# Kernel optimization log

Measured on AMD Instinct MI355X. Metric: run time of the kernel, lower is better.

The kernel has to match this reference:

```python
import math
import jax, jax.numpy as jnp
import numpy as np

FACTOR = 3  # AutoCorrelation(factor=3)

def reference(queries, keys, values):
    # queries/keys/values: [B, L, D]; source requires L == S for the broadcast below.
    B, L, D = queries.shape
    S = keys.shape[1]
    # NOTE (faithful to source): rfft is over the LAST axis with fft_length L/S,
    # i.e. the feature axis D is zero-padded (or truncated) to length L.
    q_fft = jnp.fft.rfft(queries, n=L, axis=-1)          # [B, L, L//2+1] complex
    k_fft = jnp.fft.rfft(keys, n=S, axis=-1)             # [B, S, S//2+1] complex
    corr = jnp.fft.irfft(q_fft * jnp.conj(k_fft), n=L + S - 1, axis=-1)  # [B, L, L+S-1]

    top_k = int(FACTOR * math.log(float(L)))
    mean_value = jnp.mean(corr, axis=1)                  # [B, L+S-1]
    top_k = min(top_k, mean_value.shape[-1])
    top_k_val, top_k_ind = jax.lax.top_k(mean_value, top_k)  # [B, K]
    tmp_corr = jax.nn.softmax(top_k_val, axis=-1)        # [B, K]

    # Faithful to source: the roll shift for every batch element uses the
    # delays of batch element 0 (index[0] in the TF loop).
    shifts = top_k_ind[0]                                # [K] int32
    # Vectorized replacement of the per-index tf.roll loop.
    V_rolled = jax.vmap(lambda s: jnp.roll(values, -s, axis=1))(shifts)  # [K, B, L, D]
    # Weighted aggregation over the K retained delays (intended semantics of
    # the source einsum, which as written has a rank mismatch).
    output = jnp.einsum('kbld,bk->bld', V_rolled, tmp_corr)  # [B, L, D]
    return output

def setup_inputs() -> dict:
    key = jax.random.key(0)
    k1, k2, k3 = jax.random.split(key, 3)
    B, L, D = 8, 1024, 512
    return {
        'queries': jax.random.normal(k1, (B, L, D), dtype=jnp.float32),
        'keys':    jax.random.normal(k2, (B, L, D), dtype=jnp.float32),
        'values':  jax.random.normal(k3, (B, L, D), dtype=jnp.float32),
    }
```

## Files before the change

### kernel.cpp

```cpp
#include <hip/hip_runtime.h>
#include <math.h>

#define NB 8
#define NL 1024
#define ND 512
#define NF 513
#define NT 2047
#define TOPK 20

typedef __attribute__((ext_vector_type(8))) short short8;
typedef __attribute__((ext_vector_type(4))) float f32x4;

static __device__ __forceinline__ unsigned short bf16_rne(float x) {
    unsigned int u = __builtin_bit_cast(unsigned int, x);
    unsigned int r = (u + 0x7fffu + ((u >> 16) & 1u)) >> 16;
    return (unsigned short)r;
}
static __device__ __forceinline__ float bf16_to_f(unsigned short h) {
    unsigned int u = ((unsigned int)h) << 16;
    return __builtin_bit_cast(float, u);
}

__global__ __launch_bounds__(256) void k_tr(const float* __restrict__ q,
                                            const float* __restrict__ kk,
                                            unsigned short* __restrict__ Thi,
                                            unsigned short* __restrict__ Tlo,
                                            float* __restrict__ S) {
    __shared__ float tile[64][65];
    const int which = blockIdx.z;
    const int b  = blockIdx.y;
    const int l0 = (blockIdx.x & 15) * 64;
    const int d0 = (blockIdx.x >> 4) * 64;
    const int t = threadIdx.x;
    if (which == 0 && blockIdx.x == 0) {
        for (int i = t; i < 1023; i += 256) S[b * 1023 + i] = 0.f;
    }
    const float* src = (which ? kk : q) + (size_t)b * NL * ND;
    const int r = t >> 4, c = t & 15;
    #pragma unroll
    for (int rr = 0; rr < 4; ++rr) {
        const float4 v = *(const float4*)&src[(size_t)(l0 + r + 16 * rr) * ND + d0 + c * 4];
        tile[r + 16 * rr][c * 4 + 0] = v.x;
        tile[r + 16 * rr][c * 4 + 1] = v.y;
        tile[r + 16 * rr][c * 4 + 2] = v.z;
        tile[r + 16 * rr][c * 4 + 3] = v.w;
    }
    __syncthreads();
    unsigned short* hi = Thi + ((size_t)which * NB + b) * (size_t)ND * NL;
    unsigned short* lo = Tlo + ((size_t)which * NB + b) * (size_t)ND * NL;
    #pragma unroll
    for (int p = 0; p < 2; ++p) {
        const int c2 = t + 256 * p;
        const int dl = c2 >> 3;
        const int l8 = (c2 & 7) * 8;
        short8 vh, vl;
        #pragma unroll
        for (int i = 0; i < 8; ++i) {
            const float x = tile[l8 + i][dl];
            const unsigned short h = bf16_rne(x);
            vh[i] = (short)h;
            vl[i] = (short)bf16_rne(x - bf16_to_f(h));
        }
        *(short8*)&hi[(size_t)(d0 + dl) * NL + l0 + l8] = vh;
        *(short8*)&lo[(size_t)(d0 + dl) * NL + l0 + l8] = vl;
    }
}

#define GBK 32
#define GPAD 8
#define GKT 4

__global__ __launch_bounds__(256, 3) void k_gemm(const unsigned short* __restrict__ Thi,
                                                 const unsigned short* __restrict__ Tlo,
                                                 float* __restrict__ S) {
    __shared__ unsigned short Ahi[128][GBK + GPAD];
    __shared__ unsigned short Alo[128][GBK + GPAD];
    __shared__ unsigned short Bhi[128][GBK + GPAD];
    __shared__ unsigned short Blo[128][GBK + GPAD];
    __shared__ float sd4[4][256];
    const int id   = blockIdx.x;
    const int b    = id & 7;
    const int rest = id >> 3;
    const int mt = rest & 3, nt = (rest >> 2) & 3, kq = rest >> 4;
    const int tid  = threadIdx.x;
    const int lane = tid & 63, w = tid >> 6;
    const int wr = w >> 1, wc = w & 1;
    const int m = lane & 15, g = lane >> 4;

    const size_t plane = (size_t)ND * NL;
    const unsigned short* qhi = Thi + (size_t)b * plane;
    const unsigned short* khi = Thi + ((size_t)NB + b) * plane;
    const unsigned short* qlo = Tlo + (size_t)b * plane;
    const unsigned short* klo = Tlo + ((size_t)NB + b) * plane;

    f32x4 acc[4][4];
    #pragma unroll
    for (int i = 0; i < 4; ++i)
        #pragma unroll
        for (int j = 0; j < 4; ++j) acc[i][j] = (f32x4)(0.f);

    const int kbase = kq * GKT;
    short8 r_ah[2], r_al[2], r_bh[2], r_bl[2];
    #pragma unroll
    for (int p = 0; p < 2; ++p) {
        const int cc  = tid + 256 * p;
        const int row = cc >> 2, col8 = (cc & 3) * 8;
        const size_t ga = (size_t)(mt * 128 + row) * NL + kbase * GBK + col8;
        const size_t gb = (size_t)(nt * 128 + row) * NL + kbase * GBK + col8;
        r_ah[p] = *(const short8*)&qhi[ga];
        r_al[p] = *(const short8*)&qlo[ga];
        r_bh[p] = *(const short8*)&khi[gb];
        r_bl[p] = *(const short8*)&klo[gb];
    }

    for (int kt = 0; kt < GKT; ++kt) {
        __syncthreads();
        #pragma unroll
        for (int p = 0; p < 2; ++p) {
            const int cc  = tid + 256 * p;
            const int row = cc >> 2, col8 = (cc & 3) * 8;
            *(short8*)&Ahi[row][col8] = r_ah[p];
            *(short8*)&Alo[row][col8] = r_al[p];
            *(short8*)&Bhi[row][col8] = r_bh[p];
            *(short8*)&Blo[row][col8] = r_bl[p];
        }
        __syncthreads();
        if (kt + 1 < GKT) {
            #pragma unroll
            for (int p = 0; p < 2; ++p) {
                const int cc  = tid + 256 * p;
                const int row = cc >> 2, col8 = (cc & 3) * 8;
                const size_t ga = (size_t)(mt * 128 + row) * NL + (kbase + kt + 1) * GBK + col8;
                const size_t gb = (size_t)(nt * 128 + row) * NL + (kbase + kt + 1) * GBK + col8;
                r_ah[p] = *(const short8*)&qhi[ga];
                r_al[p] = *(const short8*)&qlo[ga];
                r_bh[p] = *(const short8*)&khi[gb];
                r_bl[p] = *(const short8*)&klo[gb];
            }
        }
        short8 ah[4], al[4], bh[4], bl[4];
        #pragma unroll
        for (int i = 0; i < 4; ++i) {
            ah[i] = *(const short8*)&Ahi[wr * 64 + i * 16 + m][g * 8];
            al[i] = *(const short8*)&Alo[wr * 64 + i * 16 + m][g * 8];
        }
        #pragma unroll
        for (int j = 0; j < 4; ++j) {
            bh[j] = *(const short8*)&Bhi[wc * 64 + j * 16 + m][g * 8];
            bl[j] = *(const short8*)&Blo[wc * 64 + j * 16 + m][g * 8];
        }
        #pragma unroll
        for (int i = 0; i < 4; ++i)
            #pragma unroll
            for (int j = 0; j < 4; ++j) {
                acc[i][j] = __builtin_amdgcn_mfma_f32_16x16x32_bf16(ah[i], bh[j], acc[i][j], 0, 0, 0);
                acc[i][j] = __builtin_amdgcn_mfma_f32_16x16x32_bf16(ah[i], bl[j], acc[i][j], 0, 0, 0);
                acc[i][j] = __builtin_amdgcn_mfma_f32_16x16x32_bf16(al[i], bh[j], acc[i][j], 0, 0, 0);
            }
    }

    for (int i = tid; i < 1024; i += 256) ((float*)sd4)[i] = 0.f;
    __syncthreads();
    float bin[7][4];
    #pragma unroll
    for (int u = 0; u < 7; ++u)
        #pragma unroll
        for (int r2 = 0; r2 < 4; ++r2) bin[u][r2] = 0.f;
    #pragma unroll
    for (int i = 0; i < 4; ++i)
        #pragma unroll
        for (int j = 0; j < 4; ++j)
            #pragma unroll
            for (int r2 = 0; r2 < 4; ++r2) bin[i - j + 3][r2] += acc[i][j][r2];
    const int basei = (wr - wc) * 64 + g * 4 - m + 127;
    #pragma unroll
    for (int u = 0; u < 7; ++u)
        #pragma unroll
        for (int r2 = 0; r2 < 4; ++r2)
            atomicAdd(&sd4[w][basei + (u - 3) * 16 + r2], bin[u][r2]);
    __syncthreads();
    const int doff = (mt - nt) * 128 + 511 - 127;
    if (tid < 255) {
        const float vsum = sd4[0][tid] + sd4[1][tid] + sd4[2][tid] + sd4[3][tid];
        atomicAdd(&S[b * 1023 + doff + tid], vsum);
    }
}

__global__ __launch_bounds__(64) void k_pdft(const float* __restrict__ S,
                                             float* __restrict__ pbar) {
    const int b = blockIdx.y;
    const int f = blockIdx.x;
    const int lane = threadIdx.x;
    const float w = 2.0f * 3.14159265358979323846f / 1024.0f;
    float re = 0.f, im = 0.f;
    #pragma unroll
    for (int i = 0; i < 16; ++i) {
        const int j = lane + 64 * i;
        if (j < 1023) {
            const int mm = (f * (j - 511)) & 1023;
            float s, c;
            sincosf(w * (float)mm, &s, &c);
            const float x = S[b * 1023 + j];
            re = fmaf(x, c, re);
            im = fmaf(x, -s, im);
        }
    }
    #pragma unroll
    for (int off = 32; off; off >>= 1) {
        re += __shfl_xor(re, off);
        im += __shfl_xor(im, off);
    }
    if (lane == 0) {
        pbar[b * 2 * NF + 2 * f]     = re;
        pbar[b * 2 * NF + 2 * f + 1] = im;
    }
}

__global__ __launch_bounds__(256) void k_mean(const float* __restrict__ pbar,
                                              float* __restrict__ mv) {
    __shared__ float P[2 * NF];
    const int b = blockIdx.y;
    for (int i = threadIdx.x; i < 2 * NF; i += 256)
        P[i] = pbar[(size_t)b * (2 * NF) + i];
    __syncthreads();
    const int wave = threadIdx.x >> 6, lane = threadIdx.x & 63;
    const int t = blockIdx.x * 4 + wave;
    if (t >= NT) return;
    const float w2 = 2.0f * 3.14159265358979323846f / 2047.0f;
    float acc = 0.f;
    #pragma unroll
    for (int i = 0; i < 8; ++i) {
        const int f = 1 + lane + 64 * i;
        const int mm = (f * t) % 2047;
        float s, c;
        sincosf(w2 * (float)mm, &s, &c);
        acc = fmaf(P[2 * f], c, acc);
        acc = fmaf(-P[2 * f + 1], s, acc);
    }
    acc *= 2.0f;
    #pragma unroll
    for (int off = 32; off; off >>= 1) acc += __shfl_xor(acc, off);
    if (lane == 0)
        mv[(size_t)b * NT + t] = (acc + P[0]) * (1.0f / (2047.0f * 1024.0f));
}

__global__ __launch_bounds__(256) void k_topk(const float* __restrict__ mv,
                                              float* __restrict__ wts,
                                              int* __restrict__ shifts) {
    __shared__ float v[NT];
    __shared__ float topv[TOPK];
    __shared__ int   topi[TOPK];
    __shared__ float wv[4];
    __shared__ int   wi[4];
    const int b = blockIdx.x;
    const int t = threadIdx.x;
    const int lane = t & 63, wave = t >> 6;
    for (int i = t; i < NT; i += 256) v[i] = mv[(size_t)b * NT + i];
    __syncthreads();
    for (int kkk = 0; kkk < TOPK; ++kkk) {
        float bv = -INFINITY; int bi = 0x7fffffff;
        #pragma unroll
        for (int s = 0; s < 8; ++s) {
            const int i = t + 256 * s;
            if (i < NT) {
                const float x = v[i];
                if (x > bv) { bv = x; bi = i; }
            }
        }
        #pragma unroll
        for (int off = 32; off; off >>= 1) {
            const float ov = __shfl_down(bv, off);
            const int   oi = __shfl_down(bi, off);
            if (ov > bv || (ov == bv && oi < bi)) { bv = ov; bi = oi; }
        }
        if (lane == 0) { wv[wave] = bv; wi[wave] = bi; }
        __syncthreads();
        if (t == 0) {
            bv = wv[0]; bi = wi[0];
            #pragma unroll
            for (int ww = 1; ww < 4; ++ww)
                if (wv[ww] > bv || (wv[ww] == bv && wi[ww] < bi)) { bv = wv[ww]; bi = wi[ww]; }
            topv[kkk] = bv; topi[kkk] = bi;
            v[bi] = -INFINITY;
        }
        __syncthreads();
    }
    if (t == 0) {
        float m = topv[0], sum = 0.f, e[TOPK];
        #pragma unroll
        for (int i = 0; i < TOPK; ++i) { e[i] = expf(topv[i] - m); sum += e[i]; }
        #pragma unroll
        for (int i = 0; i < TOPK; ++i) wts[b * TOPK + i] = e[i] / sum;
        if (b == 0) {
            #pragma unroll
            for (int i = 0; i < TOPK; ++i) shifts[i] = topi[i];
        }
    }
}

__global__ __launch_bounds__(128) void k_out(const float* __restrict__ vals,
                                             const float* __restrict__ wts,
                                             const int* __restrict__ shifts,
                                             float* __restrict__ out) {
    __shared__ float w[TOPK];
    __shared__ int   sh[TOPK];
    const int id = blockIdx.x;
    const int b = id & 7;
    const int l = id >> 3;
    const int t = threadIdx.x;
    if (t < TOPK) { w[t] = wts[b * TOPK + t]; sh[t] = shifts[t]; }
    __syncthreads();
    float4 acc = make_float4(0.f, 0.f, 0.f, 0.f);
    const float4* vb = (const float4*)(vals + (size_t)b * NL * ND);
    #pragma unroll 4
    for (int kkk = 0; kkk < TOPK; ++kkk) {
        const int sl = (l + sh[kkk]) & (NL - 1);
        const float4 x = vb[(size_t)sl * (ND / 4) + t];
        const float wk = w[kkk];
        acc.x = fmaf(wk, x.x, acc.x);
        acc.y = fmaf(wk, x.y, acc.y);
        acc.z = fmaf(wk, x.z, acc.z);
        acc.w = fmaf(wk, x.w, acc.w);
    }
    ((float4*)out)[((size_t)b * NL + l) * (ND / 4) + t] = acc;
}

extern "C" void kernel_launch(void* const* d_in, const int* in_sizes, int n_in,
                              void* d_out, int out_size, void* d_ws, size_t ws_size,
                              hipStream_t stream) {
    const float* q = (const float*)d_in[0];
    const float* k = (const float*)d_in[1];
    const float* v = (const float*)d_in[2];
    float* out    = (float*)d_out;

    const size_t plane = (size_t)ND * NL;
    unsigned short* Thi = (unsigned short*)d_ws;
    unsigned short* Tlo = Thi + 2 * NB * plane;
    float* S      = (float*)(Tlo + 2 * NB * plane);
    float* pbar   = S + NB * 1023;
    float* mv     = pbar + NB * 2 * NF;
    float* wts    = mv + NB * NT;
    int*   shifts = (int*)(wts + NB * TOPK);

    k_tr  <<<dim3(128, NB, 2), 256, 0, stream>>>(q, k, Thi, Tlo, S);
    k_gemm<<<1024, 256, 0, stream>>>(Thi, Tlo, S);
    k_pdft<<<dim3(NF, NB), 64, 0, stream>>>(S, pbar);
    k_mean<<<dim3(512, NB), 256, 0, stream>>>(pbar, mv);
    k_topk<<<NB, 256, 0, stream>>>(mv, wts, shifts);
    k_out <<<NL * NB, 128, 0, stream>>>(v, wts, shifts, out);
}
```

Measured before the change: 202.7 us.

## Drop LDS staging in diagonal-sum GEMM and use per-wave direct-load tiles

Rewrites the split-bf16 correlation GEMM so each wave loads its own 64x32 tile fragments straight from global memory into MFMA registers. The shared-memory A/B staging and the block-wide barriers are gone, and the K split becomes 256 per block. The diagonal binning is now reduced per wave into a small LDS buffer and flushed with global atomics, and the occupancy hint rises to 4. This removes LDS traffic and synchronisation, but it loses cross-wave tile reuse and relies on L1/L2 for the repeated A loads. It also issues more global atomic adds.

```diff
diff --git a/kernel.cpp b/kernel.cpp
--- a/kernel.cpp
+++ b/kernel.cpp
@@ -66,26 +66,21 @@
     }
 }
 
-#define GBK 32
-#define GPAD 8
-#define GKT 4
-
-__global__ __launch_bounds__(256, 3) void k_gemm(const unsigned short* __restrict__ Thi,
+__global__ __launch_bounds__(256, 4) void k_gemm(const unsigned short* __restrict__ Thi,
                                                  const unsigned short* __restrict__ Tlo,
                                                  float* __restrict__ S) {
-    __shared__ unsigned short Ahi[128][GBK + GPAD];
-    __shared__ unsigned short Alo[128][GBK + GPAD];
-    __shared__ unsigned short Bhi[128][GBK + GPAD];
-    __shared__ unsigned short Blo[128][GBK + GPAD];
-    __shared__ float sd4[4][256];
+    __shared__ float sd[4][96];
     const int id   = blockIdx.x;
     const int b    = id & 7;
     const int rest = id >> 3;
-    const int mt = rest & 3, nt = (rest >> 2) & 3, kq = rest >> 4;
+    const int ntg  = rest & 3;
+    const int mt   = (rest >> 2) & 7;
+    const int kq   = rest >> 5;
     const int tid  = threadIdx.x;
-    const int lane = tid & 63, w = tid >> 6;
-    const int wr = w >> 1, wc = w & 1;
+    const int w = tid >> 6, lane = tid & 63;
     const int m = lane & 15, g = lane >> 4;
+    const int nt = ntg * 4 + w;
+    const int D0 = mt * 64, E0 = nt * 32;
 
     const size_t plane = (size_t)ND * NL;
     const unsigned short* qhi = Thi + (size_t)b * plane;
@@ -93,96 +88,69 @@
     const unsigned short* qlo = Tlo + (size_t)b * plane;
     const unsigned short* klo = Tlo + ((size_t)NB + b) * plane;
 
-    f32x4 acc[4][4];
+    sd[w][lane] = 0.f;
+    if (lane < 32) sd[w][64 + lane] = 0.f;
+
+    f32x4 acc[4][2];
     #pragma unroll
     for (int i = 0; i < 4; ++i)
         #pragma unroll
-        for (int j = 0; j < 4; ++j) acc[i][j] = (f32x4)(0.f);
-
-    const int kbase = kq * GKT;
-    short8 r_ah[2], r_al[2], r_bh[2], r_bl[2];
-    #pragma unroll
-    for (int p = 0; p < 2; ++p) {
-        const int cc  = tid + 256 * p;
-        const int row = cc >> 2, col8 = (cc & 3) * 8;
-        const size_t ga = (size_t)(mt * 128 + row) * NL + kbase * GBK + col8;
-        const size_t gb = (size_t)(nt * 128 + row) * NL + kbase * GBK + col8;
-        r_ah[p] = *(const short8*)&qhi[ga];
-        r_al[p] = *(const short8*)&qlo[ga];
-        r_bh[p] = *(const short8*)&khi[gb];
-        r_bl[p] = *(const short8*)&klo[gb];
-    }
-
-    for (int kt = 0; kt < GKT; ++kt) {
-        __syncthreads();
-        #pragma unroll
-        for (int p = 0; p < 2; ++p) {
-            const int cc  = tid + 256 * p;
-            const int row = cc >> 2, col8 = (cc & 3) * 8;
-            *(short8*)&Ahi[row][col8] = r_ah[p];
-            *(short8*)&Alo[row][col8] = r_al[p];
-            *(short8*)&Bhi[row][col8] = r_bh[p];
-            *(short8*)&Blo[row][col8] = r_bl[p];
-        }
-        __syncthreads();
-        if (kt + 1 < GKT) {
-            #pragma unroll
-            for (int p = 0; p < 2; ++p) {
-                const int cc  = tid + 256 * p;
-                const int row = cc >> 2, col8 = (cc & 3) * 8;
-                const size_t ga = (size_t)(mt * 128 + row) * NL + (kbase + kt + 1) * GBK + col8;
-                const size_t gb = (size_t)(nt * 128 + row) * NL + (kbase + kt + 1) * GBK + col8;
-                r_ah[p] = *(const short8*)&qhi[ga];
-                r_al[p] = *(const short8*)&qlo[ga];
-                r_bh[p] = *(const short8*)&khi[gb];
-                r_bl[p] = *(const short8*)&klo[gb];
-            }
-        }
-        short8 ah[4], al[4], bh[4], bl[4];
+        for (int j = 0; j < 2; ++j) acc[i][j] = (f32x4)(0.f);
+
+    const int k00 = kq * 256;
+    size_t ar[4], br[2];
+    #pragma unroll
+    for (int i = 0; i < 4; ++i) ar[i] = (size_t)(D0 + i * 16 + m) * NL;
+    #pragma unroll
+    for (int j = 0; j < 2; ++j) br[j] = (size_t)(E0 + j * 16 + m) * NL;
+
+    #pragma unroll
+    for (int kt = 0; kt < 8; ++kt) {
+        const int k0 = k00 + kt * 32 + g * 8;
+        short8 ah[4], al[4], bh[2], bl[2];
         #pragma unroll
         for (int i = 0; i < 4; ++i) {
-            ah[i] = *(const short8*)&Ahi[wr * 64 + i * 16 + m][g * 8];
-            al[i] = *(const short8*)&Alo[wr * 64 + i * 16 + m][g * 8];
-        }
-        #pragma unroll
-        for (int j = 0; j < 4; ++j) {
-            bh[j] = *(const short8*)&Bhi[wc * 64 + j * 16 + m][g * 8];
-            bl[j] = *(const short8*)&Blo[wc * 64 + j * 16 + m][g * 8];
+            ah[i] = *(const short8*)&qhi[ar[i] + k0];
+            al[i] = *(const short8*)&qlo[ar[i] + k0];
+        }
+        #pragma unroll
+        for (int j = 0; j < 2; ++j) {
+            bh[j] = *(const short8*)&khi[br[j] + k0];
+            bl[j] = *(const short8*)&klo[br[j] + k0];
         }
         #pragma unroll
         for (int i = 0; i < 4; ++i)
             #pragma unroll
-            for (int j = 0; j < 4; ++j) {
+            for (int j = 0; j < 2; ++j) {
                 acc[i][j] = __builtin_amdgcn_mfma_f32_16x16x32_bf16(ah[i], bh[j], acc[i][j], 0, 0, 0);
                 acc[i][j] = __builtin_amdgcn_mfma_f32_16x16x32_bf16(ah[i], bl[j], acc[i][j], 0, 0, 0);
                 acc[i][j] = __builtin_amdgcn_mfma_f32_16x16x32_bf16(al[i], bh[j], acc[i][j], 0, 0, 0);
             }
     }
 
-    for (int i = tid; i < 1024; i += 256) ((float*)sd4)[i] = 0.f;
-    __syncthreads();
-    float bin[7][4];
-    #pragma unroll
-    for (int u = 0; u < 7; ++u)
+    float bin[5][4];
+    #pragma unroll
+    for (int u = 0; u < 5; ++u)
         #pragma unroll
         for (int r2 = 0; r2 < 4; ++r2) bin[u][r2] = 0.f;
     #pragma unroll
     for (int i = 0; i < 4; ++i)
         #pragma unroll
-        for (int j = 0; j < 4; ++j)
+        for (int j = 0; j < 2; ++j)
             #pragma unroll
-            for (int r2 = 0; r2 < 4; ++r2) bin[i - j + 3][r2] += acc[i][j][r2];
-    const int basei = (wr - wc) * 64 + g * 4 - m + 127;
-    #pragma unroll
-    for (int u = 0; u < 7; ++u)
+            for (int r2 = 0; r2 < 4; ++r2) bin[i - j + 1][r2] += acc[i][j][r2];
+    const int baseidx = g * 4 - m + 15;
+    #pragma unroll
+    for (int u = 0; u < 5; ++u)
         #pragma unroll
         for (int r2 = 0; r2 < 4; ++r2)
-            atomicAdd(&sd4[w][basei + (u - 3) * 16 + r2], bin[u][r2]);
-    __syncthreads();
-    const int doff = (mt - nt) * 128 + 511 - 127;
-    if (tid < 255) {
-        const float vsum = sd4[0][tid] + sd4[1][tid] + sd4[2][tid] + sd4[3][tid];
-        atomicAdd(&S[b * 1023 + doff + tid], vsum);
+            atomicAdd(&sd[w][u * 16 + baseidx + r2], bin[u][r2]);
+    __threadfence_block();
+    const int gbase = b * 1023 + 511 + (D0 - E0) - 31;
+    #pragma unroll
+    for (int t2 = 0; t2 < 2; ++t2) {
+        const int idx = lane + 64 * t2;
+        if (idx < 95) atomicAdd(&S[gbase + idx], sd[w][idx]);
     }
 }
 
```

After: 220.6 us. 8.8% more time.
